# Kernel optimization log

Measured on AMD Instinct MI355X. Metric: run time of the kernel, lower is better.

The kernel has to match this reference:

```python
import jax, jax.numpy as jnp
import numpy as np

B, T, E, V, U = 4096, 80, 100, 10000, 1024


def setup_inputs() -> dict:
    key = jax.random.key(0)
    ks = jax.random.split(key, 8)
    def w(k, shape, fan_in):
        return jax.random.normal(k, shape, jnp.float32) * (1.0 / np.sqrt(fan_in))
    return {
        "inputs": jax.random.randint(ks[0], (B, T), 0, V, dtype=jnp.int32),
        "emb_table": w(ks[1], (V, E), E),
        "Wx0": w(ks[2], (E, U), E),
        "Wh0": w(ks[3], (U, U), U),
        "b0": jnp.zeros((U,), jnp.float32),
        "Wx1": w(ks[4], (U, U), U),
        "Wh1": w(ks[5], (U, U), U),
        "b1": jnp.zeros((U,), jnp.float32),
        "Wfc": w(ks[6], (U, 1), U),
        "bfc": jnp.zeros((1,), jnp.float32),
    }


def reference(inputs, emb_table, Wx0, Wh0, b0, Wx1, Wh1, b1, Wfc, bfc):
    # Embedding lookup: [B, T, E]
    x = emb_table[inputs]
    # Time-major for scan: [T, B, E]
    xs = jnp.swapaxes(x, 0, 1)
    h0_init = jnp.zeros((inputs.shape[0], Wh0.shape[0]), x.dtype)
    h1_init = jnp.zeros((inputs.shape[0], Wh1.shape[0]), x.dtype)

    def step(carry, xt):
        h0, h1 = carry
        # SimpleRNNCell: h' = tanh(x @ Wx + h @ Wh + b); output == new state
        h0 = jnp.tanh(xt @ Wx0 + h0 @ Wh0 + b0)
        h1 = jnp.tanh(h0 @ Wx1 + h1 @ Wh1 + b1)
        return (h0, h1), None

    (h0, h1), _ = jax.lax.scan(step, (h0_init, h1_init), xs)
    # Final dense + sigmoid on last layer-1 output
    prob = jax.nn.sigmoid(h1 @ Wfc + bfc)
    return prob
```

## Files before the change

### kernel.cpp

```cpp
#include <hip/hip_runtime.h>
#include <stdint.h>

#define B_ 4096
#define T_ 80
#define E_ 100
#define V_ 10000
#define U_ 1024

typedef unsigned short u16;
typedef __attribute__((ext_vector_type(8))) __bf16 bf16x8;
typedef __attribute__((ext_vector_type(4))) float f32x4;

__device__ __forceinline__ float bf2f(u16 u) {
    union { unsigned int i; float f; } v; v.i = ((unsigned int)u) << 16; return v.f;
}
__device__ __forceinline__ u16 f2bf(float f) {
    union { float f; unsigned int i; } v; v.f = f;
    unsigned int x = v.i;
    return (u16)((x + 0x7fffu + ((x >> 16) & 1u)) >> 16);
}

__device__ __forceinline__ void load16(const void* g, void* l) {
    __builtin_amdgcn_global_load_lds(
        (__attribute__((address_space(1))) void*)(uintptr_t)g,
        (__attribute__((address_space(3))) void*)(uint32_t)(uintptr_t)l,
        16, 0, 0);
}

__global__ void transpose_pad(const float* __restrict__ src, u16* __restrict__ dst,
                              int K, int N, int Kp)
{
    __shared__ u16 tile[32][33];
    const int k0 = blockIdx.x * 32;
    const int n0 = blockIdx.y * 32;
    const int tx = threadIdx.x & 31;
    const int ty = threadIdx.x >> 5;
#pragma unroll
    for (int i = 0; i < 4; i++) {
        int k = k0 + ty + i * 8;
        tile[ty + i * 8][tx] = (k < K) ? f2bf(src[(size_t)k * N + (n0 + tx)]) : (u16)0;
    }
    __syncthreads();
#pragma unroll
    for (int i = 0; i < 4; i++) {
        int n = n0 + ty + i * 8;
        dst[(size_t)n * Kp + (k0 + tx)] = tile[tx][ty + i * 8];
    }
}

__global__ void embed_pad(const float* __restrict__ emb, u16* __restrict__ dst)
{
    int id = blockIdx.x * 256 + threadIdx.x;
    int v = id >> 7, k = id & 127;
    dst[id] = (k < E_) ? f2bf(emb[v * E_ + k]) : (u16)0;
}

__global__ void __launch_bounds__(256, 2)
rnn_phase(const u16* __restrict__ embP, const int* __restrict__ idx,
          const u16* __restrict__ Wx0T, const u16* __restrict__ Wh0T, const float* __restrict__ b0,
          const u16* __restrict__ Wx1T, const u16* __restrict__ Wh1T, const float* __restrict__ b1,
          const u16* __restrict__ h0r, u16* __restrict__ h0w,
          const u16* __restrict__ h1r, u16* __restrict__ h1w,
          int do0, int do1)
{
    const int layer = blockIdx.y & 1;
    if (layer ? !do1 : !do0) return;

    __shared__ u16 As[2][128 * 64];
    __shared__ u16 Bs[2][128 * 64];
    const int tid  = threadIdx.x;
    const int lane = tid & 63;
    const int wave = tid >> 6;
    const int wm = wave >> 1, wn = wave & 1;
    const int m0 = blockIdx.x * 128;
    const int n0 = (blockIdx.y >> 1) * 128;

    const u16 *A1, *W1, *A2, *W2; const float* bias; u16* C; int K1; bool gather;
    if (layer == 0) { A1 = embP; W1 = Wx0T; K1 = 128;  gather = true;  A2 = h0r; W2 = Wh0T; bias = b0; C = h0w; }
    else            { A1 = h0r;  W1 = Wx1T; K1 = 1024; gather = false; A2 = h1r; W2 = Wh1T; bias = b1; C = h1w; }
    const int KB1 = K1 >> 6;
    const int TOT = KB1 + (U_ >> 6);

    const int r8 = lane >> 3;
    const int c8 = lane & 7;

    int gv[4];
    if (gather) {
#pragma unroll
        for (int cc = 0; cc < 4; cc++)
            gv[cc] = idx[(size_t)(m0 + wave * 32 + cc * 8 + r8) * T_];
    }

    const f32x4 z = {0.f, 0.f, 0.f, 0.f};
    f32x4 acc[4][4];
#pragma unroll
    for (int i = 0; i < 4; i++)
#pragma unroll
        for (int j = 0; j < 4; j++) acc[i][j] = z;

    const int l15 = lane & 15, q = lane >> 4, l7 = lane & 7;
    int offA[2][4], offB[2][4];
#pragma unroll
    for (int kk = 0; kk < 2; kk++) {
#pragma unroll
        for (int f = 0; f < 4; f++) {
            const int rA = wm * 64 + f * 16 + l15;
            const int rB = wn * 64 + f * 16 + l15;
            offA[kk][f] = rA * 64 + (((kk * 4 + q) ^ l7) * 8);
            offB[kk][f] = rB * 64 + (((kk * 4 + q) ^ l7) * 8);
        }
    }

    auto stage = [&](int u, int p) {
        u16* Ad = As[p] + wave * 2048;
        u16* Bd = Bs[p] + wave * 2048;
        if (u < KB1) {
            const int k0 = u * 64;
#pragma unroll
            for (int cc = 0; cc < 4; cc++) {
                const int row = wave * 32 + cc * 8 + r8;
                const int scw = (c8 ^ (row & 7)) * 8;
                const u16* ap = gather ? A1 + (size_t)gv[cc] * 128 + k0 + scw
                                       : A1 + (size_t)(m0 + row) * K1 + k0 + scw;
                load16(ap, Ad + cc * 512);
                load16(W1 + (size_t)(n0 + row) * K1 + k0 + scw, Bd + cc * 512);
            }
        } else {
            const int k0 = (u - KB1) * 64;
#pragma unroll
            for (int cc = 0; cc < 4; cc++) {
                const int row = wave * 32 + cc * 8 + r8;
                const int scw = (c8 ^ (row & 7)) * 8;
                load16(A2 + (size_t)(m0 + row) * U_ + k0 + scw, Ad + cc * 512);
                load16(W2 + (size_t)(n0 + row) * U_ + k0 + scw, Bd + cc * 512);
            }
        }
    };

    stage(0, 0);

#pragma unroll 1
    for (int u = 0; u < TOT; ++u) {
        const int p = u & 1;
        __syncthreads();
        if (u + 1 < TOT) stage(u + 1, p ^ 1);
#pragma unroll
        for (int kk = 0; kk < 2; kk++) {
            bf16x8 a[4], b[4];
#pragma unroll
            for (int f = 0; f < 4; f++) {
                a[f] = *reinterpret_cast<const bf16x8*>(As[p] + offA[kk][f]);
                b[f] = *reinterpret_cast<const bf16x8*>(Bs[p] + offB[kk][f]);
            }
#pragma unroll
            for (int i = 0; i < 4; i++)
#pragma unroll
                for (int j = 0; j < 4; j++)
                    acc[i][j] = __builtin_amdgcn_mfma_f32_16x16x32_bf16(a[i], b[j], acc[i][j], 0, 0, 0);
        }
    }

#pragma unroll
    for (int j = 0; j < 4; j++) {
        const int col = n0 + wn * 64 + j * 16 + l15;
        const float bv = bias[col];
#pragma unroll
        for (int i = 0; i < 4; i++) {
#pragma unroll
            for (int r = 0; r < 4; r++) {
                const int row = m0 + wm * 64 + i * 16 + (q << 2) + r;
                float x = acc[i][j][r] + bv;
                x = fminf(15.f, fmaxf(-15.f, x));
                float e = __expf(2.f * x);
                C[(size_t)row * U_ + col] = f2bf((e - 1.f) / (e + 1.f));
            }
        }
    }
}

__global__ void final_dense(const u16* __restrict__ h1, const float* __restrict__ Wfc,
                            const float* __restrict__ bfc, float* __restrict__ out)
{
    const int lane = threadIdx.x & 63;
    const int wave = threadIdx.x >> 6;
    const int row = blockIdx.x * 4 + wave;
    const u16* hp = h1 + (size_t)row * U_ + lane * 16;
    const float* wp = Wfc + lane * 16;
    float s = 0.f;
#pragma unroll
    for (int i = 0; i < 16; i++) s += bf2f(hp[i]) * wp[i];
#pragma unroll
    for (int off = 32; off; off >>= 1) s += __shfl_down(s, off);
    if (lane == 0) {
        float x = s + bfc[0];
        out[row] = 1.f / (1.f + __expf(-x));
    }
}

extern "C" void kernel_launch(void* const* d_in, const int* in_sizes, int n_in,
                              void* d_out, int out_size, void* d_ws, size_t ws_size,
                              hipStream_t stream)
{
    const int*   inputs = (const int*)d_in[0];
    const float* emb    = (const float*)d_in[1];
    const float* Wx0    = (const float*)d_in[2];
    const float* Wh0    = (const float*)d_in[3];
    const float* b0     = (const float*)d_in[4];
    const float* Wx1    = (const float*)d_in[5];
    const float* Wh1    = (const float*)d_in[6];
    const float* b1     = (const float*)d_in[7];
    const float* Wfc    = (const float*)d_in[8];
    const float* bfc    = (const float*)d_in[9];

    char* ws = (char*)d_ws;
    const size_t MB = 1 << 20;
    u16* h0b[2] = { (u16*)(ws + 0 * MB), (u16*)(ws + 8 * MB) };
    u16* h1b[2] = { (u16*)(ws + 16 * MB), (u16*)(ws + 24 * MB) };
    u16* embP = (u16*)(ws + 32 * MB);
    u16* Wx0T = (u16*)(ws + 35 * MB);
    u16* Wh0T = (u16*)(ws + 36 * MB);
    u16* Wx1T = (u16*)(ws + 38 * MB);
    u16* Wh1T = (u16*)(ws + 40 * MB);

    hipMemsetAsync(h0b[1], 0, 8 * MB, stream);
    hipMemsetAsync(h1b[1], 0, 8 * MB, stream);

    embed_pad<<<V_ * 128 / 256, 256, 0, stream>>>(emb, embP);
    transpose_pad<<<dim3(128 / 32, U_ / 32), 256, 0, stream>>>(Wx0, Wx0T, E_, U_, 128);
    transpose_pad<<<dim3(U_ / 32, U_ / 32), 256, 0, stream>>>(Wh0, Wh0T, U_, U_, U_);
    transpose_pad<<<dim3(U_ / 32, U_ / 32), 256, 0, stream>>>(Wx1, Wx1T, U_, U_, U_);
    transpose_pad<<<dim3(U_ / 32, U_ / 32), 256, 0, stream>>>(Wh1, Wh1T, U_, U_, U_);

    dim3 grid(B_ / 128, 2 * (U_ / 128));
    for (int p = 0; p <= T_; ++p) {
        const int e = p & 1;
        rnn_phase<<<grid, 256, 0, stream>>>(embP, inputs + p,
                                            Wx0T, Wh0T, b0, Wx1T, Wh1T, b1,
                                            h0b[e ^ 1], h0b[e], h1b[e], h1b[e ^ 1],
                                            (int)(p < T_), (int)(p >= 1));
    }
    final_dense<<<B_ / 4, 256, 0, stream>>>(h1b[1], Wfc, bfc, (float*)d_out);
}
```

Before: 3.001 ms.

## Pre-pack weights in MFMA fragment order and load B operands straight to registers

Replaces the weight transpose with a pack kernel that stores each 16x32 weight tile in the exact per-lane order the MFMA B operand expects. The GEMM then loads B fragments directly from global memory into registers each iteration, with no LDS staging, which halves LDS use and removes the LDS writes and reads for B. The risk is that the global B loads are issued synchronously right before the MFMAs, with no prefetch, so their latency may be exposed. Weight reuse across blocks now depends on L2 rather than LDS, and register pressure goes up.

```diff
diff --git a/kernel.cpp b/kernel.cpp
--- a/kernel.cpp
+++ b/kernel.cpp
@@ -27,25 +27,17 @@
         16, 0, 0);
 }
 
-__global__ void transpose_pad(const float* __restrict__ src, u16* __restrict__ dst,
-                              int K, int N, int Kp)
-{
-    __shared__ u16 tile[32][33];
-    const int k0 = blockIdx.x * 32;
-    const int n0 = blockIdx.y * 32;
-    const int tx = threadIdx.x & 31;
-    const int ty = threadIdx.x >> 5;
-#pragma unroll
-    for (int i = 0; i < 4; i++) {
-        int k = k0 + ty + i * 8;
-        tile[ty + i * 8][tx] = (k < K) ? f2bf(src[(size_t)k * N + (n0 + tx)]) : (u16)0;
-    }
-    __syncthreads();
-#pragma unroll
-    for (int i = 0; i < 4; i++) {
-        int n = n0 + ty + i * 8;
-        dst[(size_t)n * Kp + (k0 + tx)] = tile[tx][ty + i * 8];
-    }
+__global__ void frag_pack(const float* __restrict__ src, u16* __restrict__ dst,
+                          int K, int N, int Kp)
+{
+    const int id = blockIdx.x * 256 + threadIdx.x;
+    const int frag = id >> 9, within = id & 511;
+    const int lane = within >> 3, j = within & 7;
+    const int KPB = Kp >> 5;
+    const int n_blk = frag / KPB, k_blk = frag % KPB;
+    const int n = n_blk * 16 + (lane & 15);
+    const int k = k_blk * 32 + (lane >> 4) * 8 + j;
+    dst[id] = (k < K) ? f2bf(src[(size_t)k * N + n]) : (u16)0;
 }
 
 __global__ void embed_pad(const float* __restrict__ emb, u16* __restrict__ dst)
@@ -57,8 +49,8 @@
 
 __global__ void __launch_bounds__(256, 2)
 rnn_phase(const u16* __restrict__ embP, const int* __restrict__ idx,
-          const u16* __restrict__ Wx0T, const u16* __restrict__ Wh0T, const float* __restrict__ b0,
-          const u16* __restrict__ Wx1T, const u16* __restrict__ Wh1T, const float* __restrict__ b1,
+          const u16* __restrict__ Wx0F, const u16* __restrict__ Wh0F, const float* __restrict__ b0,
+          const u16* __restrict__ Wx1F, const u16* __restrict__ Wh1F, const float* __restrict__ b1,
           const u16* __restrict__ h0r, u16* __restrict__ h0w,
           const u16* __restrict__ h1r, u16* __restrict__ h1w,
           int do0, int do1)
@@ -67,7 +59,6 @@
     if (layer ? !do1 : !do0) return;
 
     __shared__ u16 As[2][128 * 64];
-    __shared__ u16 Bs[2][128 * 64];
     const int tid  = threadIdx.x;
     const int lane = tid & 63;
     const int wave = tid >> 6;
@@ -75,11 +66,13 @@
     const int m0 = blockIdx.x * 128;
     const int n0 = (blockIdx.y >> 1) * 128;
 
-    const u16 *A1, *W1, *A2, *W2; const float* bias; u16* C; int K1; bool gather;
-    if (layer == 0) { A1 = embP; W1 = Wx0T; K1 = 128;  gather = true;  A2 = h0r; W2 = Wh0T; bias = b0; C = h0w; }
-    else            { A1 = h0r;  W1 = Wx1T; K1 = 1024; gather = false; A2 = h1r; W2 = Wh1T; bias = b1; C = h1w; }
-    const int KB1 = K1 >> 6;
-    const int TOT = KB1 + (U_ >> 6);
+    const u16 *A1, *W1f, *A2, *W2f; const float* bias; u16* C; int K1; bool gather;
+    if (layer == 0) { A1 = embP; W1f = Wx0F; K1 = 128;  gather = true;  A2 = h0r; W2f = Wh0F; bias = b0; C = h0w; }
+    else            { A1 = h0r;  W1f = Wx1F; K1 = 1024; gather = false; A2 = h1r; W2f = Wh1F; bias = b1; C = h1w; }
+    const int KB1  = K1 >> 6;
+    const int TOT  = KB1 + (U_ >> 6);
+    const int KPB1 = K1 >> 5;
+    const int KPB2 = U_ >> 5;
 
     const int r8 = lane >> 3;
     const int c8 = lane & 7;
@@ -99,21 +92,19 @@
         for (int j = 0; j < 4; j++) acc[i][j] = z;
 
     const int l15 = lane & 15, q = lane >> 4, l7 = lane & 7;
-    int offA[2][4], offB[2][4];
-#pragma unroll
-    for (int kk = 0; kk < 2; kk++) {
+    int offA[2][4];
+#pragma unroll
+    for (int kk = 0; kk < 2; kk++)
 #pragma unroll
         for (int f = 0; f < 4; f++) {
             const int rA = wm * 64 + f * 16 + l15;
-            const int rB = wn * 64 + f * 16 + l15;
             offA[kk][f] = rA * 64 + (((kk * 4 + q) ^ l7) * 8);
-            offB[kk][f] = rB * 64 + (((kk * 4 + q) ^ l7) * 8);
-        }
-    }
+        }
+
+    const int nb = (n0 >> 4) + wn * 4;
 
     auto stage = [&](int u, int p) {
         u16* Ad = As[p] + wave * 2048;
-        u16* Bd = Bs[p] + wave * 2048;
         if (u < KB1) {
             const int k0 = u * 64;
 #pragma unroll
@@ -123,7 +114,6 @@
                 const u16* ap = gather ? A1 + (size_t)gv[cc] * 128 + k0 + scw
                                        : A1 + (size_t)(m0 + row) * K1 + k0 + scw;
                 load16(ap, Ad + cc * 512);
-                load16(W1 + (size_t)(n0 + row) * K1 + k0 + scw, Bd + cc * 512);
             }
         } else {
             const int k0 = (u - KB1) * 64;
@@ -132,7 +122,6 @@
                 const int row = wave * 32 + cc * 8 + r8;
                 const int scw = (c8 ^ (row & 7)) * 8;
                 load16(A2 + (size_t)(m0 + row) * U_ + k0 + scw, Ad + cc * 512);
-                load16(W2 + (size_t)(n0 + row) * U_ + k0 + scw, Bd + cc * 512);
             }
         }
     };
@@ -143,20 +132,30 @@
     for (int u = 0; u < TOT; ++u) {
         const int p = u & 1;
         __syncthreads();
+        bf16x8 b[2][4];
+        {
+            const u16* Wf; int kb; int KPB;
+            if (u < KB1) { Wf = W1f; kb = u * 2;          KPB = KPB1; }
+            else         { Wf = W2f; kb = (u - KB1) * 2;  KPB = KPB2; }
+#pragma unroll
+            for (int kk = 0; kk < 2; kk++)
+#pragma unroll
+                for (int f = 0; f < 4; f++)
+                    b[kk][f] = *reinterpret_cast<const bf16x8*>(
+                        Wf + ((size_t)(nb + f) * KPB + kb + kk) * 512 + lane * 8);
+        }
         if (u + 1 < TOT) stage(u + 1, p ^ 1);
 #pragma unroll
         for (int kk = 0; kk < 2; kk++) {
-            bf16x8 a[4], b[4];
-#pragma unroll
-            for (int f = 0; f < 4; f++) {
+            bf16x8 a[4];
+#pragma unroll
+            for (int f = 0; f < 4; f++)
                 a[f] = *reinterpret_cast<const bf16x8*>(As[p] + offA[kk][f]);
-                b[f] = *reinterpret_cast<const bf16x8*>(Bs[p] + offB[kk][f]);
-            }
 #pragma unroll
             for (int i = 0; i < 4; i++)
 #pragma unroll
                 for (int j = 0; j < 4; j++)
-                    acc[i][j] = __builtin_amdgcn_mfma_f32_16x16x32_bf16(a[i], b[j], acc[i][j], 0, 0, 0);
+                    acc[i][j] = __builtin_amdgcn_mfma_f32_16x16x32_bf16(a[i], b[kk][j], acc[i][j], 0, 0, 0);
         }
     }
 
@@ -217,25 +216,25 @@
     u16* h0b[2] = { (u16*)(ws + 0 * MB), (u16*)(ws + 8 * MB) };
     u16* h1b[2] = { (u16*)(ws + 16 * MB), (u16*)(ws + 24 * MB) };
     u16* embP = (u16*)(ws + 32 * MB);
-    u16* Wx0T = (u16*)(ws + 35 * MB);
-    u16* Wh0T = (u16*)(ws + 36 * MB);
-    u16* Wx1T = (u16*)(ws + 38 * MB);
-    u16* Wh1T = (u16*)(ws + 40 * MB);
+    u16* Wx0F = (u16*)(ws + 35 * MB);
+    u16* Wh0F = (u16*)(ws + 36 * MB);
+    u16* Wx1F = (u16*)(ws + 38 * MB);
+    u16* Wh1F = (u16*)(ws + 40 * MB);
 
     hipMemsetAsync(h0b[1], 0, 8 * MB, stream);
     hipMemsetAsync(h1b[1], 0, 8 * MB, stream);
 
     embed_pad<<<V_ * 128 / 256, 256, 0, stream>>>(emb, embP);
-    transpose_pad<<<dim3(128 / 32, U_ / 32), 256, 0, stream>>>(Wx0, Wx0T, E_, U_, 128);
-    transpose_pad<<<dim3(U_ / 32, U_ / 32), 256, 0, stream>>>(Wh0, Wh0T, U_, U_, U_);
-    transpose_pad<<<dim3(U_ / 32, U_ / 32), 256, 0, stream>>>(Wx1, Wx1T, U_, U_, U_);
-    transpose_pad<<<dim3(U_ / 32, U_ / 32), 256, 0, stream>>>(Wh1, Wh1T, U_, U_, U_);
+    frag_pack<<<(U_ / 16) * (128 / 32) * 512 / 256, 256, 0, stream>>>(Wx0, Wx0F, E_, U_, 128);
+    frag_pack<<<(U_ / 16) * (U_ / 32) * 512 / 256, 256, 0, stream>>>(Wh0, Wh0F, U_, U_, U_);
+    frag_pack<<<(U_ / 16) * (U_ / 32) * 512 / 256, 256, 0, stream>>>(Wx1, Wx1F, U_, U_, U_);
+    frag_pack<<<(U_ / 16) * (U_ / 32) * 512 / 256, 256, 0, stream>>>(Wh1, Wh1F, U_, U_, U_);
 
     dim3 grid(B_ / 128, 2 * (U_ / 128));
     for (int p = 0; p <= T_; ++p) {
         const int e = p & 1;
         rnn_phase<<<grid, 256, 0, stream>>>(embP, inputs + p,
-                                            Wx0T, Wh0T, b0, Wx1T, Wh1T, b1,
+                                            Wx0F, Wh0F, b0, Wx1F, Wh1F, b1,
                                             h0b[e ^ 1], h0b[e], h1b[e], h1b[e ^ 1],
                                             (int)(p < T_), (int)(p >= 1));
     }
```

After: 4.234 ms. 41.1% more time.
